# Kernel tuning notes

Hardware: AMD Instinct MI355X
Metric: run time of the kernel (lower is better)

## Reference

```python
import jax, jax.numpy as jnp
import numpy as np


def setup_inputs() -> dict:
    key = jax.random.key(0)
    k1, k2, k3 = jax.random.split(key, 3)
    B, C, D, H, W = 4, 64, 32, 64, 64
    x = jax.random.normal(k1, (B, C, D, H, W), dtype=jnp.float32)
    # Conv3d(in=2, out=1, k=7), PyTorch default init: U(-s, s), s = 1/sqrt(fan_in)
    fan_in = 2 * 7 * 7 * 7
    s = 1.0 / np.sqrt(fan_in)
    conv_w = jax.random.uniform(k2, (1, 2, 7, 7, 7), dtype=jnp.float32, minval=-s, maxval=s)
    conv_b = jax.random.uniform(k3, (1,), dtype=jnp.float32, minval=-s, maxval=s)
    return {"x": x, "conv_w": conv_w, "conv_b": conv_b}


def reference(x, conv_w, conv_b):
    # channel-wise max and mean -> [B, 2, D, H, W]
    xc = jnp.stack([jnp.max(x, axis=1), jnp.mean(x, axis=1)], axis=1)
    # conv3d 2->1, k7, stride 1, padding 3 (SAME)
    y = jax.lax.conv_general_dilated(
        xc, conv_w,
        window_strides=(1, 1, 1),
        padding=[(3, 3), (3, 3), (3, 3)],
        dimension_numbers=("NCDHW", "OIDHW", "NCDHW"),
    ) + conv_b[None, :, None, None, None]
    scale = jax.nn.sigmoid(y)  # [B, 1, D, H, W]
    return x * scale
```

## Files before the change

### kernel.cpp

```cpp
#include <hip/hip_runtime.h>
#include <math.h>

#define B_ 4
#define C_ 64
#define D_ 32
#define H_ 64
#define W_ 64
#define S_ (D_*H_*W_)
#define S4_ (S_/4)
#define HW_ (H_*W_)

typedef float floatx4 __attribute__((ext_vector_type(4)));

__global__ __launch_bounds__(256) void reduce_kernel(const float* __restrict__ x,
                                                     float* __restrict__ xc) {
    int i  = blockIdx.x * 256 + threadIdx.x;
    int b  = i >> 15;
    int s4 = i & (S4_ - 1);
    const float4* x4 = reinterpret_cast<const float4*>(x) + (size_t)b * C_ * S4_ + s4;
    float4 v = x4[0];
    float mx0 = v.x, mx1 = v.y, mx2 = v.z, mx3 = v.w;
    float sm0 = v.x, sm1 = v.y, sm2 = v.z, sm3 = v.w;
    #pragma unroll 8
    for (int c = 1; c < C_; ++c) {
        float4 t = x4[(size_t)c * S4_];
        mx0 = fmaxf(mx0, t.x); sm0 += t.x;
        mx1 = fmaxf(mx1, t.y); sm1 += t.y;
        mx2 = fmaxf(mx2, t.z); sm2 += t.z;
        mx3 = fmaxf(mx3, t.w); sm3 += t.w;
    }
    float4* o = reinterpret_cast<float4*>(xc);
    float4 a; a.x = mx0; a.y = mx1; a.z = mx2; a.w = mx3;
    o[((size_t)b * 2 + 0) * S4_ + s4] = a;
    const float inv = 1.0f / 64.0f;
    float4 m; m.x = sm0 * inv; m.y = sm1 * inv; m.z = sm2 * inv; m.w = sm3 * inv;
    o[((size_t)b * 2 + 1) * S4_ + s4] = m;
}

#define ZT 8
#define YT 14
#define XS 72
#define PLANE (YT*XS)
#define CHSZ (ZT*PLANE)
#define HALO_N (2*ZT*YT*70)

__global__ __launch_bounds__(256, 2) void conv_gate_kernel(const float* __restrict__ xc,
                                                           const float* __restrict__ x,
                                                           const float* __restrict__ cw,
                                                           const float* __restrict__ cb,
                                                           float* __restrict__ out) {
    __shared__ __align__(16) float tile[2 * CHSZ];

    const int tid = threadIdx.x;
    const int b  = blockIdx.z >> 4;
    const int d0 = (blockIdx.z & 15) * 2;
    const int h0 = blockIdx.y * 8;

    const int sw4 = tid & 15;
    const int shh = (tid >> 4) & 7;
    const int sdd = tid >> 7;

    for (int base = tid; base < HALO_N; base += 256 * 8) {
        float sv[8];
        int   sa[8];
        #pragma unroll
        for (int k = 0; k < 8; ++k) {
            int idx = base + k * 256;
            sv[k] = 0.f;
            sa[k] = -1;
            if (idx < HALO_N) {
                int ch = idx / 7840;
                int r  = idx - ch * 7840;
                int z  = r / 980;
                int r2 = r - z * 980;
                int y  = r2 / 70;
                int xw = r2 - y * 70;
                sa[k] = ch * CHSZ + z * PLANE + y * XS + xw;
                int gd = d0 + z - 3, gh = h0 + y - 3, gw = xw - 3;
                if ((unsigned)gd < (unsigned)D_ && (unsigned)gh < (unsigned)H_ &&
                    (unsigned)gw < (unsigned)W_)
                    sv[k] = xc[(size_t)(b * 2 + ch) * S_ + gd * HW_ + gh * W_ + gw];
            }
        }
        #pragma unroll
        for (int k = 0; k < 8; ++k)
            if (sa[k] >= 0) tile[sa[k]] = sv[k];
    }

    const size_t sp = (size_t)(d0 + sdd) * HW_ + (size_t)(h0 + shh) * W_ + sw4 * 4;
    const float* xp = x + (size_t)b * C_ * S_ + sp;
    float* op = out + (size_t)b * C_ * S_ + sp;
    floatx4 v0[16];
    #pragma unroll
    for (int k = 0; k < 16; ++k)
        v0[k] = *reinterpret_cast<const floatx4*>(xp + (size_t)k * S_);

    __syncthreads();

    floatx4 s0, s1;
    const int cw4 = tid & 15;
    const int chg = (tid >> 4) & 3;
    const int cdd = (tid >> 6) & 1;
    if (tid < 128) {
        float acc0[4] = {0.f, 0.f, 0.f, 0.f};
        float acc1[4] = {0.f, 0.f, 0.f, 0.f};
        for (int ch = 0; ch < 2; ++ch) {
            const float* tch = &tile[ch * CHSZ + cdd * PLANE + cw4 * 4];
            const float* wch = cw + ch * 343;
            for (int kz = 0; kz < 7; ++kz) {
                const float* trow = tch + kz * PLANE + (chg * 2) * XS;
                const float* wkz  = wch + kz * 49;
                float wp[7];
                #pragma unroll
                for (int r = 0; r < 8; ++r) {
                    const float* rp = trow + r * XS;
                    float4 f0 = *reinterpret_cast<const float4*>(rp);
                    float4 f1 = *reinterpret_cast<const float4*>(rp + 4);
                    float2 f2 = *reinterpret_cast<const float2*>(rp + 8);
                    float win[10] = {f0.x, f0.y, f0.z, f0.w,
                                     f1.x, f1.y, f1.z, f1.w, f2.x, f2.y};
                    if (r >= 1) {
                        #pragma unroll
                        for (int kw = 0; kw < 7; ++kw) {
                            acc1[0] = fmaf(win[kw + 0], wp[kw], acc1[0]);
                            acc1[1] = fmaf(win[kw + 1], wp[kw], acc1[1]);
                            acc1[2] = fmaf(win[kw + 2], wp[kw], acc1[2]);
                            acc1[3] = fmaf(win[kw + 3], wp[kw], acc1[3]);
                        }
                    }
                    if (r < 7) {
                        const float* wr = wkz + r * 7;
                        float wc[7];
                        #pragma unroll
                        for (int k = 0; k < 7; ++k) wc[k] = wr[k];
                        #pragma unroll
                        for (int kw = 0; kw < 7; ++kw) {
                            acc0[0] = fmaf(win[kw + 0], wc[kw], acc0[0]);
                            acc0[1] = fmaf(win[kw + 1], wc[kw], acc0[1]);
                            acc0[2] = fmaf(win[kw + 2], wc[kw], acc0[2]);
                            acc0[3] = fmaf(win[kw + 3], wc[kw], acc0[3]);
                        }
                        #pragma unroll
                        for (int k = 0; k < 7; ++k) wp[k] = wc[k];
                    }
                }
            }
        }
        const float bias = cb[0];
        s0.x = 1.0f / (1.0f + __expf(-(acc0[0] + bias)));
        s0.y = 1.0f / (1.0f + __expf(-(acc0[1] + bias)));
        s0.z = 1.0f / (1.0f + __expf(-(acc0[2] + bias)));
        s0.w = 1.0f / (1.0f + __expf(-(acc0[3] + bias)));
        s1.x = 1.0f / (1.0f + __expf(-(acc1[0] + bias)));
        s1.y = 1.0f / (1.0f + __expf(-(acc1[1] + bias)));
        s1.z = 1.0f / (1.0f + __expf(-(acc1[2] + bias)));
        s1.w = 1.0f / (1.0f + __expf(-(acc1[3] + bias)));
    }
    __syncthreads();

    floatx4* scl = reinterpret_cast<floatx4*>(tile);
    if (tid < 128) {
        scl[(cdd * 8 + chg * 2 + 0) * 16 + cw4] = s0;
        scl[(cdd * 8 + chg * 2 + 1) * 16 + cw4] = s1;
    }
    __syncthreads();

    const floatx4 sc = scl[(sdd * 8 + shh) * 16 + sw4];
    #pragma unroll
    for (int k = 0; k < 16; ++k)
        *reinterpret_cast<floatx4*>(op + (size_t)k * S_) = v0[k] * sc;
    for (int c = 16; c < C_; c += 8) {
        floatx4 v[8];
        #pragma unroll
        for (int k = 0; k < 8; ++k)
            v[k] = *reinterpret_cast<const floatx4*>(xp + (size_t)(c + k) * S_);
        #pragma unroll
        for (int k = 0; k < 8; ++k)
            *reinterpret_cast<floatx4*>(op + (size_t)(c + k) * S_) = v[k] * sc;
    }
}

extern "C" void kernel_launch(void* const* d_in, const int* in_sizes, int n_in,
                              void* d_out, int out_size, void* d_ws, size_t ws_size,
                              hipStream_t stream) {
    const float* x  = (const float*)d_in[0];
    const float* cw = (const float*)d_in[1];
    const float* cb = (const float*)d_in[2];
    float* out = (float*)d_out;
    float* xc  = (float*)d_ws;

    reduce_kernel<<<dim3((B_ * S4_) / 256), dim3(256), 0, stream>>>(x, xc);
    conv_gate_kernel<<<dim3(1, H_ / 8, B_ * (D_ / 2)), dim3(256), 0, stream>>>(
        xc, x, cw, cb, out);
}
```

Before: 82.48 us.

## Split fused conv+gate kernel into separate conv-scale and gate kernels

The fused conv/gate kernel becomes two kernels. The first computes only the sigmoid scale map from the halo tile and writes it to workspace. The second streams x with many more parallel threads (2048 blocks, each thread covering 16 channels) and multiplies by the scale. This is meant to fix the low parallelism of the fused kernel's streaming phase, which had only 512 blocks with half their threads idle during the conv. The cost is an extra kernel launch and a small scale-map write and read.

```diff
diff --git a/kernel.cpp b/kernel.cpp
--- a/kernel.cpp
+++ b/kernel.cpp
@@ -44,21 +44,16 @@
 #define CHSZ (ZT*PLANE)
 #define HALO_N (2*ZT*YT*70)
 
-__global__ __launch_bounds__(256, 2) void conv_gate_kernel(const float* __restrict__ xc,
-                                                           const float* __restrict__ x,
-                                                           const float* __restrict__ cw,
-                                                           const float* __restrict__ cb,
-                                                           float* __restrict__ out) {
+__global__ __launch_bounds__(256, 2) void conv_scale_kernel(const float* __restrict__ xc,
+                                                            const float* __restrict__ cw,
+                                                            const float* __restrict__ cb,
+                                                            float* __restrict__ scale) {
     __shared__ __align__(16) float tile[2 * CHSZ];
 
     const int tid = threadIdx.x;
     const int b  = blockIdx.z >> 4;
     const int d0 = (blockIdx.z & 15) * 2;
     const int h0 = blockIdx.y * 8;
-
-    const int sw4 = tid & 15;
-    const int shh = (tid >> 4) & 7;
-    const int sdd = tid >> 7;
 
     for (int base = tid; base < HALO_N; base += 256 * 8) {
         float sv[8];
@@ -86,22 +81,12 @@
         for (int k = 0; k < 8; ++k)
             if (sa[k] >= 0) tile[sa[k]] = sv[k];
     }
-
-    const size_t sp = (size_t)(d0 + sdd) * HW_ + (size_t)(h0 + shh) * W_ + sw4 * 4;
-    const float* xp = x + (size_t)b * C_ * S_ + sp;
-    float* op = out + (size_t)b * C_ * S_ + sp;
-    floatx4 v0[16];
-    #pragma unroll
-    for (int k = 0; k < 16; ++k)
-        v0[k] = *reinterpret_cast<const floatx4*>(xp + (size_t)k * S_);
-
     __syncthreads();
 
-    floatx4 s0, s1;
-    const int cw4 = tid & 15;
-    const int chg = (tid >> 4) & 3;
-    const int cdd = (tid >> 6) & 1;
     if (tid < 128) {
+        const int cw4 = tid & 15;
+        const int chg = (tid >> 4) & 3;
+        const int cdd = (tid >> 6) & 1;
         float acc0[4] = {0.f, 0.f, 0.f, 0.f};
         float acc1[4] = {0.f, 0.f, 0.f, 0.f};
         for (int ch = 0; ch < 2; ++ch) {
@@ -147,6 +132,7 @@
             }
         }
         const float bias = cb[0];
+        floatx4 s0, s1;
         s0.x = 1.0f / (1.0f + __expf(-(acc0[0] + bias)));
         s0.y = 1.0f / (1.0f + __expf(-(acc0[1] + bias)));
         s0.z = 1.0f / (1.0f + __expf(-(acc0[2] + bias)));
@@ -155,28 +141,35 @@
         s1.y = 1.0f / (1.0f + __expf(-(acc1[1] + bias)));
         s1.z = 1.0f / (1.0f + __expf(-(acc1[2] + bias)));
         s1.w = 1.0f / (1.0f + __expf(-(acc1[3] + bias)));
+        float* sp = &scale[(size_t)b * S_ + (size_t)(d0 + cdd) * HW_ +
+                           (size_t)(h0 + chg * 2) * W_ + cw4 * 4];
+        *reinterpret_cast<floatx4*>(sp)      = s0;
+        *reinterpret_cast<floatx4*>(sp + W_) = s1;
     }
-    __syncthreads();
+}
 
-    floatx4* scl = reinterpret_cast<floatx4*>(tile);
-    if (tid < 128) {
-        scl[(cdd * 8 + chg * 2 + 0) * 16 + cw4] = s0;
-        scl[(cdd * 8 + chg * 2 + 1) * 16 + cw4] = s1;
-    }
-    __syncthreads();
-
-    const floatx4 sc = scl[(sdd * 8 + shh) * 16 + sw4];
+__global__ __launch_bounds__(256) void gate_kernel(const float* __restrict__ x,
+                                                   const float* __restrict__ scale,
+                                                   float* __restrict__ out) {
+    int t = blockIdx.x * 256 + threadIdx.x;
+    int cchunk = t >> 17;
+    int pos = t & 131071;
+    int b  = pos >> 15;
+    int s4 = pos & (S4_ - 1);
+    const floatx4* xp = reinterpret_cast<const floatx4*>(x) + (size_t)b * C_ * S4_ + s4;
+    floatx4* op = reinterpret_cast<floatx4*>(out) + (size_t)b * C_ * S4_ + s4;
+    const floatx4 sc = reinterpret_cast<const floatx4*>(scale)[(size_t)b * S4_ + s4];
+    const int c0 = cchunk * 16;
     #pragma unroll
-    for (int k = 0; k < 16; ++k)
-        *reinterpret_cast<floatx4*>(op + (size_t)k * S_) = v0[k] * sc;
-    for (int c = 16; c < C_; c += 8) {
+    for (int half = 0; half < 2; ++half) {
+        const int cb_ = c0 + half * 8;
         floatx4 v[8];
         #pragma unroll
         for (int k = 0; k < 8; ++k)
-            v[k] = *reinterpret_cast<const floatx4*>(xp + (size_t)(c + k) * S_);
+            v[k] = xp[(size_t)(cb_ + k) * S4_];
         #pragma unroll
         for (int k = 0; k < 8; ++k)
-            *reinterpret_cast<floatx4*>(op + (size_t)(c + k) * S_) = v[k] * sc;
+            op[(size_t)(cb_ + k) * S4_] = v[k] * sc;
     }
 }
 
@@ -186,10 +179,12 @@
     const float* x  = (const float*)d_in[0];
     const float* cw = (const float*)d_in[1];
     const float* cb = (const float*)d_in[2];
-    float* out = (float*)d_out;
-    float* xc  = (float*)d_ws;
+    float* out   = (float*)d_out;
+    float* xc    = (float*)d_ws;
+    float* scale = xc + (size_t)B_ * 2 * S_;
 
     reduce_kernel<<<dim3((B_ * S4_) / 256), dim3(256), 0, stream>>>(x, xc);
-    conv_gate_kernel<<<dim3(1, H_ / 8, B_ * (D_ / 2)), dim3(256), 0, stream>>>(
-        xc, x, cw, cb, out);
+    conv_scale_kernel<<<dim3(1, H_ / 8, B_ * (D_ / 2)), dim3(256), 0, stream>>>(
+        xc, cw, cb, scale);
+    gate_kernel<<<dim3(2048), dim3(256), 0, stream>>>(x, scale, out);
 }
```

Measured after the change: 94.56 us. 14.6% more time.
